# Kernel optimization log

Hardware: AMD Instinct MI355X
Metric: run time of the kernel (lower is better)

## Reference

```python
import jax, jax.numpy as jnp
import numpy as np

NEG = -10000.0


def _build_label_vocab():
    vocab = {'O': 0}
    i = 1
    for t in ['PER', 'ORG', 'LOC', 'MISC']:
        for p in ['B', 'I', 'E', 'S']:
            vocab[f'{p}-{t}'] = i
            i += 1
    return vocab


def _init_transition(key):
    """Random transition with BIOES constraints, matching CRF.initialize()."""
    vocab = _build_label_vocab()
    L = len(vocab) + 2          # 19 (17 labels + start + end)
    start, end = L - 2, L - 1
    T = np.array(jax.random.normal(key, (L, L)), dtype=np.float32)
    T[:, end] = NEG
    T[start, :] = NEG
    for lf, i_f in vocab.items():
        pf, tf = ('O', 'O') if lf == 'O' else lf.split('-')
        for lt, i_t in vocab.items():
            pt, tt = ('O', 'O') if lt == 'O' else lt.split('-')
            allowed = (pf in ('O', 'E', 'S') and pt in ('O', 'B', 'S')) or \
                      (pf in ('B', 'I') and pt in ('I', 'E') and tf == tt)
            if not allowed:
                T[i_t, i_f] = NEG
    return jnp.asarray(T)


def setup_inputs() -> dict:
    key = jax.random.key(0)
    k1, k2, k3, k4 = jax.random.split(key, 4)
    B, S, NL = 4096, 256, 17
    logits = jax.random.normal(k1, (B, S, NL), dtype=jnp.float32)
    labels = jax.random.randint(k2, (B, S), 0, NL)
    lens = jax.random.randint(k3, (B,), 1, S + 1)   # lengths in [1, S]
    transition = _init_transition(k4)                # [19, 19]
    return {"logits": logits, "labels": labels, "lens": lens,
            "transition": transition}


def reference(logits, labels, lens, transition):
    """CRF log-likelihood: gold_score(pad_logits(logits)) - norm_score."""
    B, S, NL = logits.shape
    L = transition.shape[0]       # label_size = NL + 2
    start, end = L - 2, L - 1

    # pad_logits: append start/end columns with -10000
    pads = jnp.full((B, S, 2), NEG, dtype=logits.dtype)
    logits_p = jnp.concatenate([logits, pads], axis=2)   # [B, S, L]

    tmask = (jnp.arange(S)[None, :] < lens[:, None])     # [B, S] valid tokens

    # ---- gold score ----
    # unary: gather emission score of the gold label at each position
    unary = jnp.take_along_axis(logits_p, labels[:, :, None], axis=2)[:, :, 0]
    unary = (unary * tmask.astype(logits.dtype)).sum(axis=1)

    # binary: transition scores along the gold path (with start/end padding)
    labels_ext = jnp.concatenate(
        [jnp.full((B, 1), start, labels.dtype), labels,
         jnp.full((B, 1), end, labels.dtype)], axis=1)   # [B, S+2]
    emask = jnp.arange(S + 2)[None, :] < (lens + 1)[:, None]
    labels_ext = jnp.where(emask, labels_ext, end)
    trn_scr = transition[labels_ext[:, 1:], labels_ext[:, :-1]]  # [B, S+1]
    bmask = (jnp.arange(S + 1)[None, :] < (lens + 1)[:, None]).astype(logits.dtype)
    binary = (trn_scr * bmask).sum(axis=1)

    gold = unary + binary

    # ---- partition (norm) score: forward algorithm over time ----
    alpha0 = jnp.full((B, L), NEG, dtype=logits.dtype).at[:, start].set(0.0)

    def step(alpha, xs):
        logit, m = xs  # logit: [B, L], m: [B] bool (position < len)
        # alpha_nxt[b,i] = logit[b,i] + LSE_j(alpha[b,j] + T[i,j])
        nxt = logit + jax.nn.logsumexp(alpha[:, None, :] + transition[None], axis=2)
        alpha = jnp.where(m[:, None], nxt, alpha)
        return alpha, None

    alpha, _ = jax.lax.scan(step, alpha0,
                            (jnp.swapaxes(logits_p, 0, 1), tmask.T))
    alpha = alpha + transition[end][None, :]
    norm = jax.nn.logsumexp(alpha, axis=1)

    return gold - norm   # [B] per-sequence log-likelihood
```

## Files before the change

### kernel.cpp

```cpp
#include <hip/hip_runtime.h>

constexpr int S   = 256;
constexpr int NL  = 17;
constexpr int L   = 19;
constexpr int WPB = 2;

__global__ __launch_bounds__(64 * WPB)
void crf_fwd(const float* __restrict__ logits,
             const int*   __restrict__ labels,
             const int*   __restrict__ lens,
             const float* __restrict__ transition,
             float* __restrict__ out, int totalElemM1)
{
    __shared__ float Tsh[L * L];
    __shared__ __align__(16) float pbuf[WPB][2][2][32];

    const int tid  = threadIdx.x;
    const int wave = tid >> 6;
    const int wtid = tid & 63;
    const int half = wtid >> 5;
    const int lane = wtid & 31;
    const int b    = blockIdx.x * WPB + wave;

    for (int k = tid; k < L * L; k += 64 * WPB) Tsh[k] = transition[k];
    __syncthreads();

    const int  i    = lane;
    const bool act  = (i < L);
    const bool emit = (i < NL);
    const int  ic   = act ? i : 0;

    float coef[L];
    #pragma unroll
    for (int j = 0; j < L; ++j)
        coef[j] = __expf(half ? Tsh[j * L + ic] : Tsh[ic * L + j]);

    const int len = lens[b];
    const int mid = len >> 1;
    const int nb  = len - 1 - mid;
    const int nup = half ? nb : mid;
    const int nsteps = (mid + 7) & ~7;

    const int seqbase = b * (S * NL);

    float p = act ? __expf(half ? Tsh[(L - 1) * L + ic]
                                : Tsh[ic * L + (L - 2)])
                  : 0.0f;
    float m = 0.0f;

    const char* lgbase = (const char*)logits;
    const int capHiF = 4 * min(seqbase + (S - 1) * NL + i, totalElemM1);
    const int capHi  = half ? 0x7ffffffc : capHiF;
    const int capLo  = half ? 4 * (seqbase + i) : 0;
    const int stride = half ? -(8 * NL * 4) : (8 * NL * 4);

    int   off[8];
    float lgbuf[8];
    #pragma unroll
    for (int u = 0; u < 8; ++u) {
        int tok = half ? (len - 1 - u) : u;
        tok = tok > 0 ? tok : 0;
        int o = 4 * (seqbase + tok * NL + i);
        o = min(o, capHiF);
        off[u] = o;
        lgbuf[u] = *(const float*)(lgbase + o);
    }

    for (int tb = 0; tb < nsteps; tb += 8) {
        #pragma unroll
        for (int u = 0; u < 8; ++u) {
            const int   t  = tb + u;
            const float lg = lgbuf[u];
            int o = off[u] + stride;
            o = max(o, capLo);
            o = min(o, capHi);
            off[u] = o;
            lgbuf[u] = *(const float*)(lgbase + o);

            const bool upd = (t < nup);

            const float el = emit ? __expf(lg) : 0.0f;
            const float pe = p * el;

            float* pb = &pbuf[wave][half][u & 1][0];
            pb[i] = pe;
            asm volatile("" ::: "memory");
            const float4* q = (const float4*)pb;
            const float4 q0 = q[0], q1 = q[1], q2 = q[2], q3 = q[3], q4 = q[4];

            float a0 = q0.x * coef[0];
            float a1 = q0.y * coef[1];
            float a2 = q0.z * coef[2];
            float a3 = q0.w * coef[3];
            a0 = fmaf(q1.x, coef[4],  a0);
            a1 = fmaf(q1.y, coef[5],  a1);
            a2 = fmaf(q1.z, coef[6],  a2);
            a3 = fmaf(q1.w, coef[7],  a3);
            a0 = fmaf(q2.x, coef[8],  a0);
            a1 = fmaf(q2.y, coef[9],  a1);
            a2 = fmaf(q2.z, coef[10], a2);
            a3 = fmaf(q2.w, coef[11], a3);
            a0 = fmaf(q3.x, coef[12], a0);
            a1 = fmaf(q3.y, coef[13], a1);
            a2 = fmaf(q3.z, coef[14], a2);
            a3 = fmaf(q3.w, coef[15], a3);
            a0 = fmaf(q4.x, coef[16], a0);
            a1 = fmaf(q4.y, coef[17], a1);
            a2 = fmaf(q4.z, coef[18], a2);

            float pn = (a0 + a1) + (a2 + a3);

            if ((u & 3) == 3) {
                float m0 = fmaxf(fmaxf(q0.x, q0.y), fmaxf(q0.z, q0.w));
                float m1 = fmaxf(fmaxf(q1.x, q1.y), fmaxf(q1.z, q1.w));
                float m2 = fmaxf(fmaxf(q2.x, q2.y), fmaxf(q2.z, q2.w));
                float m3 = fmaxf(fmaxf(q3.x, q3.y), fmaxf(q3.z, q3.w));
                float m4 = fmaxf(fmaxf(q4.x, q4.y), q4.z);
                float mx = fmaxf(fmaxf(m0, m1), fmaxf(fmaxf(m2, m3), m4));
                pn *= __frcp_rn(mx);
                m += upd ? __logf(mx) : 0.0f;
            }
            p = upd ? pn : p;
        }
    }

    {
        float lgf = 0.0f;
        if (half && emit) lgf = logits[(size_t)(seqbase + mid * NL + i)];
        if (half) p = emit ? p * __expf(lgf) : 0.0f;
    }

    const float other = __shfl_xor(p, 32);
    float prod = act ? p * other : 0.0f;
    #pragma unroll
    for (int o = 16; o >= 1; o >>= 1) prod += __shfl_xor(prod, o, 32);
    const float mtot = m + __shfl_xor(m, 32);
    const float norm = mtot + __logf(prod);

    const int* labp = labels + b * S;
    float gsum = 0.0f;
    for (int c = 0; c < len; c += 64) {
        const int tok = c + wtid;
        if (tok < len) {
            const int lab = labp[tok];
            const int prv = (tok == 0) ? (L - 2) : labp[tok - 1];
            gsum += logits[(size_t)(seqbase + tok * NL + lab)] + Tsh[lab * L + prv];
        }
    }
    #pragma unroll
    for (int o = 32; o >= 1; o >>= 1) gsum += __shfl_xor(gsum, o);
    const float gold = gsum + Tsh[(L - 1) * L + labp[len - 1]];

    if (wtid == 0) out[b] = gold - norm;
}

extern "C" void kernel_launch(void* const* d_in, const int* in_sizes, int n_in,
                              void* d_out, int out_size, void* d_ws, size_t ws_size,
                              hipStream_t stream)
{
    (void)n_in; (void)out_size; (void)d_ws; (void)ws_size;
    const float* logits     = (const float*)d_in[0];
    const int*   labels     = (const int*)d_in[1];
    const int*   lens       = (const int*)d_in[2];
    const float* transition = (const float*)d_in[3];
    float*       out        = (float*)d_out;
    const int B = in_sizes[2];
    const int totalElemM1 = B * S * NL - 1;
    crf_fwd<<<dim3(B / WPB), dim3(64 * WPB), 0, stream>>>(
        logits, labels, lens, transition, out, totalElemM1);
}
```

Baseline: 136.1 us.

## Rewrite CRF forward as per-thread sequence chains with sparse transition constants

Replaces the wave-per-sequence design, where each lane held one label and exchanged values through LDS, with a design where each thread owns a whole sequence and keeps all 17 label states in registers. The forward and backward half-chains now run in separate blocks of a single kernel, and a second combine kernel handles the meet-in-the-middle product and the gold score. Transitions forbidden by BIOES are dropped at compile time, which removes their FMAs. The cost is heavy register use, only 128 blocks of 64 threads for B=4096, which leaves most CUs idle, an extra kernel launch, and uncoalesced per-thread loads of 68-byte rows. It also hardcodes the BIOES mask, so it is only correct when the transition matrix has exactly that structure.

```diff
diff --git a/kernel.cpp b/kernel.cpp
--- a/kernel.cpp
+++ b/kernel.cpp
@@ -1,141 +1,185 @@
 #include <hip/hip_runtime.h>
 
-constexpr int S   = 256;
-constexpr int NL  = 17;
-constexpr int L   = 19;
-constexpr int WPB = 2;
-
-__global__ __launch_bounds__(64 * WPB)
-void crf_fwd(const float* __restrict__ logits,
-             const int*   __restrict__ labels,
-             const int*   __restrict__ lens,
-             const float* __restrict__ transition,
-             float* __restrict__ out, int totalElemM1)
-{
-    __shared__ float Tsh[L * L];
-    __shared__ __align__(16) float pbuf[WPB][2][2][32];
-
-    const int tid  = threadIdx.x;
-    const int wave = tid >> 6;
-    const int wtid = tid & 63;
-    const int half = wtid >> 5;
-    const int lane = wtid & 31;
-    const int b    = blockIdx.x * WPB + wave;
-
-    for (int k = tid; k < L * L; k += 64 * WPB) Tsh[k] = transition[k];
-    __syncthreads();
-
-    const int  i    = lane;
-    const bool act  = (i < L);
-    const bool emit = (i < NL);
-    const int  ic   = act ? i : 0;
-
-    float coef[L];
-    #pragma unroll
-    for (int j = 0; j < L; ++j)
-        coef[j] = __expf(half ? Tsh[j * L + ic] : Tsh[ic * L + j]);
-
-    const int len = lens[b];
+constexpr int S    = 256;
+constexpr int NL   = 17;
+constexpr int L    = 19;
+constexpr int CAPB = 16384;
+
+typedef float v4 __attribute__((ext_vector_type(4), aligned(4)));
+
+__device__ float g_Z[CAPB * 17];
+__device__ float g_V[CAPB * 17];
+__device__ float g_mf[CAPB];
+__device__ float g_mv[CAPB];
+
+__host__ __device__ constexpr bool allowedTo(int i, int j) {
+    const int pi = (i == 0) ? 4 : ((i - 1) & 3);
+    const int pj = (j == 0) ? 4 : ((j - 1) & 3);
+    const int ti = (i == 0) ? -1 : ((i - 1) >> 2);
+    const int tj = (j == 0) ? -2 : ((j - 1) >> 2);
+    const bool fromOES = (pj == 4) || (pj == 2) || (pj == 3);
+    const bool toOBS   = (pi == 4) || (pi == 0) || (pi == 3);
+    if (fromOES && toOBS) return true;
+    if (((pj == 0) || (pj == 1)) && ((pi == 1) || (pi == 2)) && (ti == tj)) return true;
+    return false;
+}
+
+#define STEP(T_, CUR, NXT, RN)                                              \
+    {                                                                       \
+        const int t_ = (T_);                                                \
+        {                                                                   \
+            const int o_ = tokoff(t_ + 1);                                  \
+            const v4   l0 = *(const v4*)(base + o_);                        \
+            const v4   l1 = *(const v4*)(base + o_ + 16);                   \
+            const v4   l2 = *(const v4*)(base + o_ + 32);                   \
+            const v4   l3 = *(const v4*)(base + o_ + 48);                   \
+            const float l4 = *(const float*)(base + o_ + 64);               \
+            NXT[0] = l0.x;  NXT[1] = l0.y;  NXT[2] = l0.z;  NXT[3] = l0.w;  \
+            NXT[4] = l1.x;  NXT[5] = l1.y;  NXT[6] = l1.z;  NXT[7] = l1.w;  \
+            NXT[8] = l2.x;  NXT[9] = l2.y;  NXT[10] = l2.z; NXT[11] = l2.w; \
+            NXT[12] = l3.x; NXT[13] = l3.y; NXT[14] = l3.z; NXT[15] = l3.w; \
+            NXT[16] = l4;                                                   \
+        }                                                                   \
+        float q[17];                                                        \
+        _Pragma("unroll")                                                   \
+        for (int j = 0; j < 17; ++j) q[j] = __expf(CUR[j]) * p[j];          \
+        _Pragma("unroll")                                                   \
+        for (int i = 0; i < 17; ++i) {                                      \
+            float acc = 0.0f;                                               \
+            bool  fst = true;                                               \
+            _Pragma("unroll")                                               \
+            for (int j = 0; j < 17; ++j) {                                  \
+                const bool al = BWD ? allowedTo(j, i) : allowedTo(i, j);    \
+                if (al) {                                                   \
+                    acc = fst ? cf[i][j] * q[j]                             \
+                              : fmaf(cf[i][j], q[j], acc);                  \
+                    fst = false;                                            \
+                }                                                           \
+            }                                                               \
+            p[i] = acc;                                                     \
+        }                                                                   \
+        if (RN) {                                                           \
+            float mx = p[16];                                               \
+            _Pragma("unroll")                                               \
+            for (int i = 0; i < 16; i += 2)                                 \
+                mx = fmaxf(mx, fmaxf(p[i], p[i + 1]));                      \
+            const float r_ = __frcp_rn(mx);                                 \
+            _Pragma("unroll")                                               \
+            for (int i = 0; i < 17; ++i) p[i] *= r_;                        \
+            m += __logf(mx);                                                \
+        }                                                                   \
+        if (t_ == nup - 1) {                                                \
+            float* dst = SC + bc * 17;                                      \
+            _Pragma("unroll")                                               \
+            for (int i = 0; i < 17; ++i) dst[i] = p[i];                     \
+            SM[bc] = m;                                                     \
+        }                                                                   \
+    }
+
+template <bool BWD>
+__device__ __forceinline__ void chain(const float* __restrict__ logits,
+                                      const int*   __restrict__ lens,
+                                      const float* __restrict__ T,
+                                      int B, int z)
+{
+    const int  lane  = threadIdx.x;
+    const int  braw  = z * 64 + lane;
+    const bool valid = braw < B;
+    const int  bc    = valid ? braw : 0;
+
+    const int len = lens[bc];
     const int mid = len >> 1;
-    const int nb  = len - 1 - mid;
-    const int nup = half ? nb : mid;
-    const int nsteps = (mid + 7) & ~7;
-
-    const int seqbase = b * (S * NL);
-
-    float p = act ? __expf(half ? Tsh[(L - 1) * L + ic]
-                                : Tsh[ic * L + (L - 2)])
-                  : 0.0f;
+    int nup = BWD ? (len - 1 - mid) : mid;
+    if (!valid) nup = 0;
+
+    float cf[17][17];
+    #pragma unroll
+    for (int i = 0; i < 17; ++i)
+        #pragma unroll
+        for (int j = 0; j < 17; ++j) {
+            const bool al = BWD ? allowedTo(j, i) : allowedTo(i, j);
+            if (al) cf[i][j] = __expf(BWD ? T[j * L + i] : T[i * L + j]);
+        }
+
+    float p[17];
+    #pragma unroll
+    for (int i = 0; i < 17; ++i)
+        p[i] = __expf(BWD ? T[(L - 1) * L + i] : T[i * L + (L - 2)]);
+
     float m = 0.0f;
 
-    const char* lgbase = (const char*)logits;
-    const int capHiF = 4 * min(seqbase + (S - 1) * NL + i, totalElemM1);
-    const int capHi  = half ? 0x7ffffffc : capHiF;
-    const int capLo  = half ? 4 * (seqbase + i) : 0;
-    const int stride = half ? -(8 * NL * 4) : (8 * NL * 4);
-
-    int   off[8];
-    float lgbuf[8];
-    #pragma unroll
-    for (int u = 0; u < 8; ++u) {
-        int tok = half ? (len - 1 - u) : u;
-        tok = tok > 0 ? tok : 0;
-        int o = 4 * (seqbase + tok * NL + i);
-        o = min(o, capHiF);
-        off[u] = o;
-        lgbuf[u] = *(const float*)(lgbase + o);
-    }
-
-    for (int tb = 0; tb < nsteps; tb += 8) {
+    float* SC = BWD ? g_V : g_Z;
+    float* SM = BWD ? g_mv : g_mf;
+
+    if (nup == 0 && valid) {
+        float* dst = SC + bc * 17;
         #pragma unroll
-        for (int u = 0; u < 8; ++u) {
-            const int   t  = tb + u;
-            const float lg = lgbuf[u];
-            int o = off[u] + stride;
-            o = max(o, capLo);
-            o = min(o, capHi);
-            off[u] = o;
-            lgbuf[u] = *(const float*)(lgbase + o);
-
-            const bool upd = (t < nup);
-
-            const float el = emit ? __expf(lg) : 0.0f;
-            const float pe = p * el;
-
-            float* pb = &pbuf[wave][half][u & 1][0];
-            pb[i] = pe;
-            asm volatile("" ::: "memory");
-            const float4* q = (const float4*)pb;
-            const float4 q0 = q[0], q1 = q[1], q2 = q[2], q3 = q[3], q4 = q[4];
-
-            float a0 = q0.x * coef[0];
-            float a1 = q0.y * coef[1];
-            float a2 = q0.z * coef[2];
-            float a3 = q0.w * coef[3];
-            a0 = fmaf(q1.x, coef[4],  a0);
-            a1 = fmaf(q1.y, coef[5],  a1);
-            a2 = fmaf(q1.z, coef[6],  a2);
-            a3 = fmaf(q1.w, coef[7],  a3);
-            a0 = fmaf(q2.x, coef[8],  a0);
-            a1 = fmaf(q2.y, coef[9],  a1);
-            a2 = fmaf(q2.z, coef[10], a2);
-            a3 = fmaf(q2.w, coef[11], a3);
-            a0 = fmaf(q3.x, coef[12], a0);
-            a1 = fmaf(q3.y, coef[13], a1);
-            a2 = fmaf(q3.z, coef[14], a2);
-            a3 = fmaf(q3.w, coef[15], a3);
-            a0 = fmaf(q4.x, coef[16], a0);
-            a1 = fmaf(q4.y, coef[17], a1);
-            a2 = fmaf(q4.z, coef[18], a2);
-
-            float pn = (a0 + a1) + (a2 + a3);
-
-            if ((u & 3) == 3) {
-                float m0 = fmaxf(fmaxf(q0.x, q0.y), fmaxf(q0.z, q0.w));
-                float m1 = fmaxf(fmaxf(q1.x, q1.y), fmaxf(q1.z, q1.w));
-                float m2 = fmaxf(fmaxf(q2.x, q2.y), fmaxf(q2.z, q2.w));
-                float m3 = fmaxf(fmaxf(q3.x, q3.y), fmaxf(q3.z, q3.w));
-                float m4 = fmaxf(fmaxf(q4.x, q4.y), q4.z);
-                float mx = fmaxf(fmaxf(m0, m1), fmaxf(fmaxf(m2, m3), m4));
-                pn *= __frcp_rn(mx);
-                m += upd ? __logf(mx) : 0.0f;
-            }
-            p = upd ? pn : p;
-        }
-    }
-
+        for (int i = 0; i < 17; ++i) dst[i] = p[i];
+        SM[bc] = 0.0f;
+    }
+
+    int nmax = nup;
+    #pragma unroll
+    for (int o = 32; o >= 1; o >>= 1) nmax = max(nmax, __shfl_xor(nmax, o));
+
+    const char* base = (const char*)logits;
+    const int   sb4  = bc * (S * NL * 4);
+
+    auto tokoff = [&](int t) -> int {
+        int tok = BWD ? (len - 1 - t) : t;
+        if (BWD) tok = tok > 0 ? tok : 0;
+        return sb4 + tok * (NL * 4);
+    };
+
+    float curv[17], nxtv[17];
     {
-        float lgf = 0.0f;
-        if (half && emit) lgf = logits[(size_t)(seqbase + mid * NL + i)];
-        if (half) p = emit ? p * __expf(lgf) : 0.0f;
-    }
-
-    const float other = __shfl_xor(p, 32);
-    float prod = act ? p * other : 0.0f;
-    #pragma unroll
-    for (int o = 16; o >= 1; o >>= 1) prod += __shfl_xor(prod, o, 32);
-    const float mtot = m + __shfl_xor(m, 32);
-    const float norm = mtot + __logf(prod);
+        const int o_ = tokoff(0);
+        const v4   l0 = *(const v4*)(base + o_);
+        const v4   l1 = *(const v4*)(base + o_ + 16);
+        const v4   l2 = *(const v4*)(base + o_ + 32);
+        const v4   l3 = *(const v4*)(base + o_ + 48);
+        const float l4 = *(const float*)(base + o_ + 64);
+        curv[0] = l0.x;  curv[1] = l0.y;  curv[2] = l0.z;  curv[3] = l0.w;
+        curv[4] = l1.x;  curv[5] = l1.y;  curv[6] = l1.z;  curv[7] = l1.w;
+        curv[8] = l2.x;  curv[9] = l2.y;  curv[10] = l2.z; curv[11] = l2.w;
+        curv[12] = l3.x; curv[13] = l3.y; curv[14] = l3.z; curv[15] = l3.w;
+        curv[16] = l4;
+    }
+
+    for (int tb = 0; tb < nmax; tb += 2) {
+        STEP(tb,     curv, nxtv, false)
+        STEP(tb + 1, nxtv, curv, ((tb & 3) == 2))
+    }
+}
+
+__global__ __launch_bounds__(64, 1)
+void crf_chain(const float* __restrict__ logits, const int* __restrict__ lens,
+               const float* __restrict__ T, int B, int nbh)
+{
+    if ((int)blockIdx.x < nbh) chain<false>(logits, lens, T, B, blockIdx.x);
+    else                       chain<true >(logits, lens, T, B, blockIdx.x - nbh);
+}
+
+__global__ __launch_bounds__(64)
+void crf_combine(const float* __restrict__ logits, const int* __restrict__ labels,
+                 const int* __restrict__ lens, const float* __restrict__ T,
+                 float* __restrict__ out, int B)
+{
+    const int b    = blockIdx.x;
+    const int wtid = threadIdx.x;
+    const int len  = lens[b];
+    const int mid  = len >> 1;
+
+    float prod = 0.0f;
+    if (wtid < 17) {
+        const float z  = g_Z[b * 17 + wtid];
+        const float v  = g_V[b * 17 + wtid];
+        const float lg = logits[(size_t)b * (S * NL) + mid * NL + wtid];
+        prod = z * v * __expf(lg);
+    }
+    #pragma unroll
+    for (int o = 32; o >= 1; o >>= 1) prod += __shfl_xor(prod, o);
+    const float norm = g_mf[b] + g_mv[b] + __logf(prod);
 
     const int* labp = labels + b * S;
     float gsum = 0.0f;
@@ -144,12 +188,12 @@
         if (tok < len) {
             const int lab = labp[tok];
             const int prv = (tok == 0) ? (L - 2) : labp[tok - 1];
-            gsum += logits[(size_t)(seqbase + tok * NL + lab)] + Tsh[lab * L + prv];
+            gsum += logits[(size_t)b * (S * NL) + tok * NL + lab] + T[lab * L + prv];
         }
     }
     #pragma unroll
     for (int o = 32; o >= 1; o >>= 1) gsum += __shfl_xor(gsum, o);
-    const float gold = gsum + Tsh[(L - 1) * L + labp[len - 1]];
+    const float gold = gsum + T[(L - 1) * L + labp[len - 1]];
 
     if (wtid == 0) out[b] = gold - norm;
 }
@@ -164,8 +208,9 @@
     const int*   lens       = (const int*)d_in[2];
     const float* transition = (const float*)d_in[3];
     float*       out        = (float*)d_out;
-    const int B = in_sizes[2];
-    const int totalElemM1 = B * S * NL - 1;
-    crf_fwd<<<dim3(B / WPB), dim3(64 * WPB), 0, stream>>>(
-        logits, labels, lens, transition, out, totalElemM1);
-}
+    const int B   = in_sizes[2];
+    const int NBH = (B + 63) / 64;
+
+    crf_chain<<<dim3(2 * NBH), dim3(64), 0, stream>>>(logits, lens, transition, B, NBH);
+    crf_combine<<<dim3(B), dim3(64), 0, stream>>>(logits, labels, lens, transition, out, B);
+}
```

Measured after the change: 166.5 us. +22.4%, slower.
